# Performance work log

Hardware: AMD Instinct MI355X
Metric: run time of the kernel (lower is better)

## Reference

```python
import jax, jax.numpy as jnp
import numpy as np

B, T, C = 4, 2048, 1024
H = 16
HD = C // H  # 64


def setup_inputs() -> dict:
    key = jax.random.key(0)
    ks = jax.random.split(key, 5)
    x = jax.random.normal(ks[0], (B, T, C), dtype=jnp.float32)
    # torch nn.Linear weights have shape [out_features, in_features]
    s = 1.0 / np.sqrt(C)
    Wq = jax.random.uniform(ks[1], (C, C), jnp.float32, -s, s)
    Wk = jax.random.uniform(ks[2], (C, C), jnp.float32, -s, s)
    Wv = jax.random.uniform(ks[3], (C, C), jnp.float32, -s, s)
    Wo = jax.random.uniform(ks[4], (C, C), jnp.float32, -s, s)
    return {"x": x, "Wq": Wq, "Wk": Wk, "Wv": Wv, "Wo": Wo}


def _split_heads(t):
    b, s, c = t.shape
    return t.reshape(b, s, H, HD).transpose(0, 2, 1, 3)  # [B,H,T,HD]


def reference(x, Wq, Wk, Wv, Wo):
    q = _split_heads(x @ Wq.T)
    k = _split_heads(x @ Wk.T)
    v = _split_heads(x @ Wv.T)
    scale = 1.0 / np.sqrt(HD).astype(np.float32)
    scores = jnp.einsum('bhqd,bhkd->bhqk', q, k) * scale  # [B,H,T,T]
    causal = jnp.tril(jnp.ones((T, T), dtype=bool))
    scores = jnp.where(causal[None, None], scores, -jnp.inf)
    weights = jax.nn.softmax(scores, axis=-1)
    ctx = jnp.einsum('bhqk,bhkd->bhqd', weights, v)
    y = ctx.transpose(0, 2, 1, 3).reshape(x.shape[0], x.shape[1], C)
    return y @ Wo.T
```

## Files before the change

kernel.cpp:

```cpp
#include <hip/hip_runtime.h>

typedef __attribute__((ext_vector_type(8))) short short8;
typedef __attribute__((ext_vector_type(4))) float floatx4;

__device__ __forceinline__ ushort f2bf(float f) {
  unsigned u = __float_as_uint(f);
  u += 0x7fffu + ((u >> 16) & 1u);
  return (ushort)(u >> 16);
}

__device__ __forceinline__ uint2 pack4(floatx4 v, float scale) {
  unsigned p0 = __float_as_uint(v[0] * scale) + 0x8000u;
  unsigned p1 = __float_as_uint(v[1] * scale) + 0x8000u;
  unsigned p2 = __float_as_uint(v[2] * scale) + 0x8000u;
  unsigned p3 = __float_as_uint(v[3] * scale) + 0x8000u;
  uint2 w;
  w.x = __builtin_amdgcn_perm(p1, p0, 0x07060302);
  w.y = __builtin_amdgcn_perm(p3, p2, 0x07060302);
  return w;
}

__device__ __forceinline__ void gll16(const ushort* g, ushort* l) {
  __builtin_amdgcn_global_load_lds(
      (const __attribute__((address_space(1))) unsigned int*)(g),
      (__attribute__((address_space(3))) unsigned int*)(l), 16, 0, 0);
}

__global__ void cvt_all(const float* __restrict__ x, const float* __restrict__ a,
                        const float* __restrict__ b, const float* __restrict__ c,
                        const float* __restrict__ d, ushort* __restrict__ ox,
                        ushort* __restrict__ oa, ushort* __restrict__ ob,
                        ushort* __restrict__ oc, ushort* __restrict__ od) {
  int bid = blockIdx.x;
  const float* in;
  ushort* out;
  int lb;
  if (bid < 8192) { in = x; out = ox; lb = bid; }
  else {
    int w = (bid - 8192) >> 10;
    lb = (bid - 8192) & 1023;
    in = w == 0 ? a : (w == 1 ? b : (w == 2 ? c : d));
    out = w == 0 ? oa : (w == 1 ? ob : (w == 2 ? oc : od));
  }
  int i = (lb * 256 + threadIdx.x) * 4;
  float4 v = *(const float4*)(in + i);
  ushort4 o = make_ushort4(f2bf(v.x), f2bf(v.y), f2bf(v.z), f2bf(v.w));
  *(ushort4*)(out + i) = o;
}

__device__ __forceinline__ void stage64(const ushort* __restrict__ G, size_t gstride,
                                        int grow0, int gcol0, ushort* __restrict__ S,
                                        int wave, int lane) {
  int r8 = lane >> 3;
  int sc = ((lane & 7) ^ (r8 & 7)) * 8;
  for (int c = 0; c < 4; c++) {
    int rl = wave * 32 + c * 8;
    gll16(&G[(size_t)(grow0 + rl + r8) * gstride + gcol0 + sc], &S[rl * 64]);
  }
}

__global__ __launch_bounds__(256) void gemm_qk(const ushort* __restrict__ A,
                                               const ushort* __restrict__ W0,
                                               const ushort* __restrict__ W1,
                                               ushort* __restrict__ Qb,
                                               ushort* __restrict__ Kb) {
  __shared__ __align__(16) ushort sA[128 * 64];
  __shared__ __align__(16) ushort sB[128 * 64];
  const int K = 1024;
  int tid = threadIdx.x, wave = tid >> 6, lane = tid & 63;
  int ln = lane & 15, quad = lane >> 4;
  int m0 = blockIdx.y * 128;
  int n0g = blockIdx.x * 128;
  int mat = n0g >> 10;
  int n0 = n0g & 1023;
  const ushort* Bw = mat == 0 ? W0 : W1;

  floatx4 acc[4][4];
  for (int i = 0; i < 4; i++)
    for (int t = 0; t < 4; t++) acc[i][t] = (floatx4)0.0f;
  int mrow = (wave >> 1) * 64, ncol = (wave & 1) * 64;

  for (int k0 = 0; k0 < K; k0 += 64) {
    __syncthreads();
    stage64(A, K, m0, k0, sA, wave, lane);
    stage64(Bw, K, n0, k0, sB, wave, lane);
    __syncthreads();
    for (int ks = 0; ks < 2; ks++) {
      int cs = ((ks * 4 + quad) ^ (ln & 7)) * 8;
      short8 af[4], bf[4];
      for (int i = 0; i < 4; i++) af[i] = *(const short8*)&sB[(ncol + i * 16 + ln) * 64 + cs];
      for (int t = 0; t < 4; t++) bf[t] = *(const short8*)&sA[(mrow + t * 16 + ln) * 64 + cs];
      for (int i = 0; i < 4; i++)
        for (int t = 0; t < 4; t++)
          acc[i][t] = __builtin_amdgcn_mfma_f32_16x16x32_bf16(af[i], bf[t], acc[i][t], 0, 0, 0);
    }
  }

  float qs = (mat == 0) ? 0.18033688f : 1.0f;
  ushort* dst = (mat == 0) ? Qb : Kb;
  for (int i = 0; i < 4; i++) {
    for (int t = 0; t < 4; t++) {
      int n = n0 + ncol + i * 16 + quad * 4;
      int m = m0 + mrow + t * 16 + ln;
      int b = m >> 11, tt = m & 2047, h = n >> 6, hd = n & 63;
      *(uint2*)&dst[((((size_t)b * 16 + h) * 2048 + tt) << 6) + hd] = pack4(acc[i][t], qs);
    }
  }
}

__global__ __launch_bounds__(256) void gemm_v(const ushort* __restrict__ A,
                                              const ushort* __restrict__ W2,
                                              ushort* __restrict__ VT) {
  __shared__ __align__(16) ushort sA[128 * 64];
  __shared__ __align__(16) ushort sB[128 * 64];
  const int K = 1024;
  int tid = threadIdx.x, wave = tid >> 6, lane = tid & 63;
  int ln = lane & 15, quad = lane >> 4;
  int m0 = blockIdx.y * 128;
  int n0 = blockIdx.x * 128;

  floatx4 acc[4][4];
  for (int i = 0; i < 4; i++)
    for (int t = 0; t < 4; t++) acc[i][t] = (floatx4)0.0f;
  int mrow = (wave >> 1) * 64, ncol = (wave & 1) * 64;

  for (int k0 = 0; k0 < K; k0 += 64) {
    __syncthreads();
    stage64(A, K, m0, k0, sA, wave, lane);
    stage64(W2, K, n0, k0, sB, wave, lane);
    __syncthreads();
    for (int ks = 0; ks < 2; ks++) {
      int cs = ((ks * 4 + quad) ^ (ln & 7)) * 8;
      short8 af[4], bf[4];
      for (int i = 0; i < 4; i++) af[i] = *(const short8*)&sA[(mrow + i * 16 + ln) * 64 + cs];
      for (int t = 0; t < 4; t++) bf[t] = *(const short8*)&sB[(ncol + t * 16 + ln) * 64 + cs];
      for (int i = 0; i < 4; i++)
        for (int t = 0; t < 4; t++)
          acc[i][t] = __builtin_amdgcn_mfma_f32_16x16x32_bf16(af[i], bf[t], acc[i][t], 0, 0, 0);
    }
  }

  for (int i = 0; i < 4; i++) {
    for (int t = 0; t < 4; t++) {
      int m = m0 + mrow + i * 16 + quad * 4;
      int n = n0 + ncol + t * 16 + ln;
      int b = m >> 11, tt = m & 2047, h = n >> 6, hd = n & 63;
      *(uint2*)&VT[(((size_t)b * 16 + h) * 64 + hd) * 2048 + tt] = pack4(acc[i][t], 1.0f);
    }
  }
}

__global__ __launch_bounds__(256) void gemm_out(const ushort* __restrict__ A,
                                                const ushort* __restrict__ W0,
                                                float* __restrict__ Fout) {
  __shared__ __align__(16) ushort sA[128 * 64];
  __shared__ __align__(16) ushort sB[128 * 64];
  const int K = 1024;
  int tid = threadIdx.x, wave = tid >> 6, lane = tid & 63;
  int ln = lane & 15, quad = lane >> 4;
  int m0 = blockIdx.y * 128;
  int n0 = blockIdx.x * 128;

  floatx4 acc[4][4];
  for (int i = 0; i < 4; i++)
    for (int t = 0; t < 4; t++) acc[i][t] = (floatx4)0.0f;
  int mrow = (wave >> 1) * 64, ncol = (wave & 1) * 64;

  for (int k0 = 0; k0 < K; k0 += 64) {
    __syncthreads();
    stage64(A, K, m0, k0, sA, wave, lane);
    stage64(W0, K, n0, k0, sB, wave, lane);
    __syncthreads();
    for (int ks = 0; ks < 2; ks++) {
      int cs = ((ks * 4 + quad) ^ (ln & 7)) * 8;
      short8 af[4], bf[4];
      for (int i = 0; i < 4; i++) af[i] = *(const short8*)&sB[(ncol + i * 16 + ln) * 64 + cs];
      for (int t = 0; t < 4; t++) bf[t] = *(const short8*)&sA[(mrow + t * 16 + ln) * 64 + cs];
      for (int i = 0; i < 4; i++)
        for (int t = 0; t < 4; t++)
          acc[i][t] = __builtin_amdgcn_mfma_f32_16x16x32_bf16(af[i], bf[t], acc[i][t], 0, 0, 0);
    }
  }

  for (int i = 0; i < 4; i++) {
    for (int t = 0; t < 4; t++) {
      int n = n0 + ncol + i * 16 + quad * 4;
      int m = m0 + mrow + t * 16 + ln;
      *(floatx4*)&Fout[(size_t)m * 1024 + n] = acc[i][t];
    }
  }
}

#define SD 76
__global__ __launch_bounds__(256) void attn(const ushort* __restrict__ Qb,
                                            const ushort* __restrict__ Kb,
                                            const ushort* __restrict__ VTb,
                                            ushort* __restrict__ ctx) {
  __shared__ __align__(16) ushort sK[64 * 64];
  __shared__ __align__(16) ushort sVT[64 * 64];
  __shared__ __align__(16) ushort sP[128 * SD];

  int tid = threadIdx.x, wave = tid >> 6, lane = tid & 63;
  int ln = lane & 15, quad = lane >> 4;
  int bh = blockIdx.x;
  int qb = 15 - blockIdx.y;

  const ushort* Qp = Qb + (size_t)bh * 2048 * 64 + (size_t)qb * 128 * 64;
  const ushort* Kp = Kb + (size_t)bh * 2048 * 64;
  const ushort* VTp = VTb + (size_t)bh * 64 * 2048;

  for (int i = 0; i < 4; i++) {
    int e = tid + i * 256;
    int row = e >> 3, c8 = (e & 7) * 8;
    *(uint4*)&sP[row * SD + c8] = *(const uint4*)&Qp[row * 64 + c8];
  }
  __syncthreads();
  short8 qf[2][2];
  for (int f = 0; f < 2; f++)
    for (int ks = 0; ks < 2; ks++)
      qf[f][ks] = *(const short8*)&sP[(wave * 32 + f * 16 + ln) * SD + ks * 32 + quad * 8];

  floatx4 o[2][4];
  for (int f = 0; f < 2; f++)
    for (int t = 0; t < 4; t++) o[f][t] = (floatx4)0.0f;
  float l_acc[2] = {0.0f, 0.0f};

  int kt_m = 2 * qb + (wave >> 1);
  int ktend = 2 * qb + 1;
  int r8 = lane >> 3;
  int scs = ((lane & 7) ^ (r8 & 7)) * 8;

  for (int kt = 0; kt <= ktend; kt++) {
    __syncthreads();
    for (int c = 0; c < 2; c++) {
      int rl = wave * 16 + c * 8;
      gll16(&Kp[(size_t)(kt * 64 + rl + r8) * 64 + scs], &sK[rl * 64]);
      gll16(&VTp[(size_t)(rl + r8) * 2048 + kt * 64 + scs], &sVT[rl * 64]);
    }
    __syncthreads();
    if (kt > kt_m) continue;

    floatx4 s[2][4];
    for (int f = 0; f < 2; f++)
      for (int t = 0; t < 4; t++) s[f][t] = (floatx4)0.0f;
    for (int ks = 0; ks < 2; ks++) {
      int cs = ((ks * 4 + quad) ^ (ln & 7)) * 8;
      short8 kf[4];
      for (int t = 0; t < 4; t++)
        kf[t] = *(const short8*)&sK[(t * 16 + ln) * 64 + cs];
      for (int f = 0; f < 2; f++)
        for (int t = 0; t < 4; t++)
          s[f][t] = __builtin_amdgcn_mfma_f32_16x16x32_bf16(kf[t], qf[f][ks], s[f][t], 0, 0, 0);
    }

    if (kt == kt_m) {
      for (int f = 0; f < 2; f++) {
        int qg = qb * 128 + wave * 32 + f * 16 + ln;
        for (int t = 0; t < 4; t++) {
          int kg = kt * 64 + t * 16 + quad * 4;
          for (int r = 0; r < 4; r++)
            if (kg + r > qg) s[f][t][r] = -1e30f;
        }
      }
    }

    for (int f = 0; f < 2; f++) {
      int prow = (wave * 32 + f * 16 + ln) * SD;
      for (int t = 0; t < 4; t++) {
        floatx4 p;
        for (int r = 0; r < 4; r++) {
          p[r] = __builtin_amdgcn_exp2f(s[f][t][r]);
          l_acc[f] += p[r];
        }
        *(uint2*)&sP[prow + t * 16 + quad * 4] = pack4(p, 1.0f);
      }
    }

    for (int ks = 0; ks < 2; ks++) {
      int cs = ((ks * 4 + quad) ^ (ln & 7)) * 8;
      short8 vf[4];
      for (int t = 0; t < 4; t++)
        vf[t] = *(const short8*)&sVT[(t * 16 + ln) * 64 + cs];
      for (int f = 0; f < 2; f++) {
        short8 pf = *(const short8*)&sP[(wave * 32 + f * 16 + ln) * SD + ks * 32 + quad * 8];
        for (int t = 0; t < 4; t++)
          o[f][t] = __builtin_amdgcn_mfma_f32_16x16x32_bf16(pf, vf[t], o[f][t], 0, 0, 0);
      }
    }
  }

  for (int f = 0; f < 2; f++) {
    l_acc[f] += __shfl_xor(l_acc[f], 16);
    l_acc[f] += __shfl_xor(l_acc[f], 32);
  }

  int b = bh >> 4, h = bh & 15;
  for (int f = 0; f < 2; f++) {
    for (int r = 0; r < 4; r++) {
      float lr = __shfl(l_acc[f], quad * 4 + r);
      float linv = 1.0f / lr;
      int qg = qb * 128 + wave * 32 + f * 16 + quad * 4 + r;
      for (int t = 0; t < 4; t++) {
        int col = h * 64 + t * 16 + ln;
        ctx[((size_t)b * 2048 + qg) * 1024 + col] = f2bf(o[f][t][r] * linv);
      }
    }
  }
}

extern "C" void kernel_launch(void* const* d_in, const int* in_sizes, int n_in,
                              void* d_out, int out_size, void* d_ws, size_t ws_size,
                              hipStream_t stream) {
  const float* x  = (const float*)d_in[0];
  const float* Wq = (const float*)d_in[1];
  const float* Wk = (const float*)d_in[2];
  const float* Wv = (const float*)d_in[3];
  const float* Wo = (const float*)d_in[4];
  float* out = (float*)d_out;

  char* ws = (char*)d_ws;
  const size_t MB = 1024 * 1024;
  ushort* xb   = (ushort*)(ws + 0);
  ushort* Wqb  = (ushort*)(ws + 16 * MB);
  ushort* Wkb  = (ushort*)(ws + 18 * MB);
  ushort* Wvb  = (ushort*)(ws + 20 * MB);
  ushort* Wob  = (ushort*)(ws + 22 * MB);
  ushort* Qb   = (ushort*)(ws + 24 * MB);
  ushort* Kb   = (ushort*)(ws + 40 * MB);
  ushort* Vtb  = (ushort*)(ws + 56 * MB);
  ushort* ctxb = xb;

  cvt_all<<<12288, 256, 0, stream>>>(x, Wq, Wk, Wv, Wo, xb, Wqb, Wkb, Wvb, Wob);

  gemm_qk<<<dim3(16, 64), 256, 0, stream>>>(xb, Wqb, Wkb, Qb, Kb);
  gemm_v<<<dim3(8, 64), 256, 0, stream>>>(xb, Wvb, Vtb);
  attn<<<dim3(64, 16), 256, 0, stream>>>(Qb, Kb, Vtb, ctxb);
  gemm_out<<<dim3(8, 64), 256, 0, stream>>>(ctxb, Wob, out);
}
```

Before: 263.6 us.

## Merge QK and V projections into one kernel and remap block scheduling

Fuses the Q/K and V projection GEMMs into a single launch that picks the weight matrix and output layout per block. All grids become 1D, with the M index varying fastest so blocks running together share weight tiles. The attention grid is remapped so consecutive blocks alternate long and short causal query tiles across heads, to balance load across CUs. This saves one launch and the tail gap between kernels, at the cost of a runtime branch on the operand pointers and the epilogue.

```diff
diff --git a/kernel.cpp b/kernel.cpp
--- a/kernel.cpp
+++ b/kernel.cpp
@@ -59,31 +59,96 @@
   }
 }
 
-__global__ __launch_bounds__(256) void gemm_qk(const ushort* __restrict__ A,
-                                               const ushort* __restrict__ W0,
-                                               const ushort* __restrict__ W1,
-                                               ushort* __restrict__ Qb,
-                                               ushort* __restrict__ Kb) {
+__global__ __launch_bounds__(256) void gemm_qkv(const ushort* __restrict__ A,
+                                                const ushort* __restrict__ W0,
+                                                const ushort* __restrict__ W1,
+                                                const ushort* __restrict__ W2,
+                                                ushort* __restrict__ Qb,
+                                                ushort* __restrict__ Kb,
+                                                ushort* __restrict__ VT) {
   __shared__ __align__(16) ushort sA[128 * 64];
   __shared__ __align__(16) ushort sB[128 * 64];
   const int K = 1024;
   int tid = threadIdx.x, wave = tid >> 6, lane = tid & 63;
   int ln = lane & 15, quad = lane >> 4;
-  int m0 = blockIdx.y * 128;
-  int n0g = blockIdx.x * 128;
-  int mat = n0g >> 10;
-  int n0 = n0g & 1023;
-  const ushort* Bw = mat == 0 ? W0 : W1;
+  int bid = blockIdx.x;
+  int mblk = bid & 63, nblk = bid >> 6;
+  int m0 = mblk * 128;
+  int mat = nblk >> 3;
+  int n0 = (nblk & 7) * 128;
+  const ushort* Bw = mat == 0 ? W0 : (mat == 1 ? W1 : W2);
+  bool qkpath = (mat < 2);
 
   floatx4 acc[4][4];
   for (int i = 0; i < 4; i++)
     for (int t = 0; t < 4; t++) acc[i][t] = (floatx4)0.0f;
   int mrow = (wave >> 1) * 64, ncol = (wave & 1) * 64;
 
+  const ushort* PA = qkpath ? sB : sA;
+  const ushort* PB = qkpath ? sA : sB;
+  int aoff = qkpath ? ncol : mrow;
+  int boff = qkpath ? mrow : ncol;
+
   for (int k0 = 0; k0 < K; k0 += 64) {
     __syncthreads();
     stage64(A, K, m0, k0, sA, wave, lane);
     stage64(Bw, K, n0, k0, sB, wave, lane);
+    __syncthreads();
+    for (int ks = 0; ks < 2; ks++) {
+      int cs = ((ks * 4 + quad) ^ (ln & 7)) * 8;
+      short8 af[4], bf[4];
+      for (int i = 0; i < 4; i++) af[i] = *(const short8*)&PA[(aoff + i * 16 + ln) * 64 + cs];
+      for (int t = 0; t < 4; t++) bf[t] = *(const short8*)&PB[(boff + t * 16 + ln) * 64 + cs];
+      for (int i = 0; i < 4; i++)
+        for (int t = 0; t < 4; t++)
+          acc[i][t] = __builtin_amdgcn_mfma_f32_16x16x32_bf16(af[i], bf[t], acc[i][t], 0, 0, 0);
+    }
+  }
+
+  if (qkpath) {
+    float qs = (mat == 0) ? 0.18033688f : 1.0f;
+    ushort* dst = (mat == 0) ? Qb : Kb;
+    for (int i = 0; i < 4; i++) {
+      for (int t = 0; t < 4; t++) {
+        int n = n0 + ncol + i * 16 + quad * 4;
+        int m = m0 + mrow + t * 16 + ln;
+        int b = m >> 11, tt = m & 2047, h = n >> 6, hd = n & 63;
+        *(uint2*)&dst[((((size_t)b * 16 + h) * 2048 + tt) << 6) + hd] = pack4(acc[i][t], qs);
+      }
+    }
+  } else {
+    for (int i = 0; i < 4; i++) {
+      for (int t = 0; t < 4; t++) {
+        int m = m0 + mrow + i * 16 + quad * 4;
+        int n = n0 + ncol + t * 16 + ln;
+        int b = m >> 11, tt = m & 2047, h = n >> 6, hd = n & 63;
+        *(uint2*)&VT[(((size_t)b * 16 + h) * 64 + hd) * 2048 + tt] = pack4(acc[i][t], 1.0f);
+      }
+    }
+  }
+}
+
+__global__ __launch_bounds__(256) void gemm_out(const ushort* __restrict__ A,
+                                                const ushort* __restrict__ W0,
+                                                float* __restrict__ Fout) {
+  __shared__ __align__(16) ushort sA[128 * 64];
+  __shared__ __align__(16) ushort sB[128 * 64];
+  const int K = 1024;
+  int tid = threadIdx.x, wave = tid >> 6, lane = tid & 63;
+  int ln = lane & 15, quad = lane >> 4;
+  int bid = blockIdx.x;
+  int m0 = (bid & 63) * 128;
+  int n0 = (bid >> 6) * 128;
+
+  floatx4 acc[4][4];
+  for (int i = 0; i < 4; i++)
+    for (int t = 0; t < 4; t++) acc[i][t] = (floatx4)0.0f;
+  int mrow = (wave >> 1) * 64, ncol = (wave & 1) * 64;
+
+  for (int k0 = 0; k0 < K; k0 += 64) {
+    __syncthreads();
+    stage64(A, K, m0, k0, sA, wave, lane);
+    stage64(W0, K, n0, k0, sB, wave, lane);
     __syncthreads();
     for (int ks = 0; ks < 2; ks++) {
       int cs = ((ks * 4 + quad) ^ (ln & 7)) * 8;
@@ -96,92 +161,6 @@
     }
   }
 
-  float qs = (mat == 0) ? 0.18033688f : 1.0f;
-  ushort* dst = (mat == 0) ? Qb : Kb;
-  for (int i = 0; i < 4; i++) {
-    for (int t = 0; t < 4; t++) {
-      int n = n0 + ncol + i * 16 + quad * 4;
-      int m = m0 + mrow + t * 16 + ln;
-      int b = m >> 11, tt = m & 2047, h = n >> 6, hd = n & 63;
-      *(uint2*)&dst[((((size_t)b * 16 + h) * 2048 + tt) << 6) + hd] = pack4(acc[i][t], qs);
-    }
-  }
-}
-
-__global__ __launch_bounds__(256) void gemm_v(const ushort* __restrict__ A,
-                                              const ushort* __restrict__ W2,
-                                              ushort* __restrict__ VT) {
-  __shared__ __align__(16) ushort sA[128 * 64];
-  __shared__ __align__(16) ushort sB[128 * 64];
-  const int K = 1024;
-  int tid = threadIdx.x, wave = tid >> 6, lane = tid & 63;
-  int ln = lane & 15, quad = lane >> 4;
-  int m0 = blockIdx.y * 128;
-  int n0 = blockIdx.x * 128;
-
-  floatx4 acc[4][4];
-  for (int i = 0; i < 4; i++)
-    for (int t = 0; t < 4; t++) acc[i][t] = (floatx4)0.0f;
-  int mrow = (wave >> 1) * 64, ncol = (wave & 1) * 64;
-
-  for (int k0 = 0; k0 < K; k0 += 64) {
-    __syncthreads();
-    stage64(A, K, m0, k0, sA, wave, lane);
-    stage64(W2, K, n0, k0, sB, wave, lane);
-    __syncthreads();
-    for (int ks = 0; ks < 2; ks++) {
-      int cs = ((ks * 4 + quad) ^ (ln & 7)) * 8;
-      short8 af[4], bf[4];
-      for (int i = 0; i < 4; i++) af[i] = *(const short8*)&sA[(mrow + i * 16 + ln) * 64 + cs];
-      for (int t = 0; t < 4; t++) bf[t] = *(const short8*)&sB[(ncol + t * 16 + ln) * 64 + cs];
-      for (int i = 0; i < 4; i++)
-        for (int t = 0; t < 4; t++)
-          acc[i][t] = __builtin_amdgcn_mfma_f32_16x16x32_bf16(af[i], bf[t], acc[i][t], 0, 0, 0);
-    }
-  }
-
-  for (int i = 0; i < 4; i++) {
-    for (int t = 0; t < 4; t++) {
-      int m = m0 + mrow + i * 16 + quad * 4;
-      int n = n0 + ncol + t * 16 + ln;
-      int b = m >> 11, tt = m & 2047, h = n >> 6, hd = n & 63;
-      *(uint2*)&VT[(((size_t)b * 16 + h) * 64 + hd) * 2048 + tt] = pack4(acc[i][t], 1.0f);
-    }
-  }
-}
-
-__global__ __launch_bounds__(256) void gemm_out(const ushort* __restrict__ A,
-                                                const ushort* __restrict__ W0,
-                                                float* __restrict__ Fout) {
-  __shared__ __align__(16) ushort sA[128 * 64];
-  __shared__ __align__(16) ushort sB[128 * 64];
-  const int K = 1024;
-  int tid = threadIdx.x, wave = tid >> 6, lane = tid & 63;
-  int ln = lane & 15, quad = lane >> 4;
-  int m0 = blockIdx.y * 128;
-  int n0 = blockIdx.x * 128;
-
-  floatx4 acc[4][4];
-  for (int i = 0; i < 4; i++)
-    for (int t = 0; t < 4; t++) acc[i][t] = (floatx4)0.0f;
-  int mrow = (wave >> 1) * 64, ncol = (wave & 1) * 64;
-
-  for (int k0 = 0; k0 < K; k0 += 64) {
-    __syncthreads();
-    stage64(A, K, m0, k0, sA, wave, lane);
-    stage64(W0, K, n0, k0, sB, wave, lane);
-    __syncthreads();
-    for (int ks = 0; ks < 2; ks++) {
-      int cs = ((ks * 4 + quad) ^ (ln & 7)) * 8;
-      short8 af[4], bf[4];
-      for (int i = 0; i < 4; i++) af[i] = *(const short8*)&sB[(ncol + i * 16 + ln) * 64 + cs];
-      for (int t = 0; t < 4; t++) bf[t] = *(const short8*)&sA[(mrow + t * 16 + ln) * 64 + cs];
-      for (int i = 0; i < 4; i++)
-        for (int t = 0; t < 4; t++)
-          acc[i][t] = __builtin_amdgcn_mfma_f32_16x16x32_bf16(af[i], bf[t], acc[i][t], 0, 0, 0);
-    }
-  }
-
   for (int i = 0; i < 4; i++) {
     for (int t = 0; t < 4; t++) {
       int n = n0 + ncol + i * 16 + quad * 4;
@@ -202,8 +181,11 @@
 
   int tid = threadIdx.x, wave = tid >> 6, lane = tid & 63;
   int ln = lane & 15, quad = lane >> 4;
-  int bh = blockIdx.x;
-  int qb = 15 - blockIdx.y;
+  int bid = blockIdx.x;
+  int r = bid & 7, j = bid >> 3;
+  int zi = j & 15;
+  int qb = (zi & 1) ? (zi >> 1) : (15 - (zi >> 1));
+  int bh = (j >> 4) * 8 + r;
 
   const ushort* Qp = Qb + (size_t)bh * 2048 * 64 + (size_t)qb * 128 * 64;
   const ushort* Kp = Kb + (size_t)bh * 2048 * 64;
@@ -258,8 +240,8 @@
         int qg = qb * 128 + wave * 32 + f * 16 + ln;
         for (int t = 0; t < 4; t++) {
           int kg = kt * 64 + t * 16 + quad * 4;
-          for (int r = 0; r < 4; r++)
-            if (kg + r > qg) s[f][t][r] = -1e30f;
+          for (int r2 = 0; r2 < 4; r2++)
+            if (kg + r2 > qg) s[f][t][r2] = -1e30f;
         }
       }
     }
@@ -268,9 +250,9 @@
       int prow = (wave * 32 + f * 16 + ln) * SD;
       for (int t = 0; t < 4; t++) {
         floatx4 p;
-        for (int r = 0; r < 4; r++) {
-          p[r] = __builtin_amdgcn_exp2f(s[f][t][r]);
-          l_acc[f] += p[r];
+        for (int r2 = 0; r2 < 4; r2++) {
+          p[r2] = __builtin_amdgcn_exp2f(s[f][t][r2]);
+          l_acc[f] += p[r2];
         }
         *(uint2*)&sP[prow + t * 16 + quad * 4] = pack4(p, 1.0f);
       }
@@ -296,13 +278,13 @@
 
   int b = bh >> 4, h = bh & 15;
   for (int f = 0; f < 2; f++) {
-    for (int r = 0; r < 4; r++) {
-      float lr = __shfl(l_acc[f], quad * 4 + r);
+    for (int r2 = 0; r2 < 4; r2++) {
+      float lr = __shfl(l_acc[f], quad * 4 + r2);
       float linv = 1.0f / lr;
-      int qg = qb * 128 + wave * 32 + f * 16 + quad * 4 + r;
+      int qg = qb * 128 + wave * 32 + f * 16 + quad * 4 + r2;
       for (int t = 0; t < 4; t++) {
         int col = h * 64 + t * 16 + ln;
-        ctx[((size_t)b * 2048 + qg) * 1024 + col] = f2bf(o[f][t][r] * linv);
+        ctx[((size_t)b * 2048 + qg) * 1024 + col] = f2bf(o[f][t][r2] * linv);
       }
     }
   }
@@ -332,8 +314,7 @@
 
   cvt_all<<<12288, 256, 0, stream>>>(x, Wq, Wk, Wv, Wo, xb, Wqb, Wkb, Wvb, Wob);
 
-  gemm_qk<<<dim3(16, 64), 256, 0, stream>>>(xb, Wqb, Wkb, Qb, Kb);
-  gemm_v<<<dim3(8, 64), 256, 0, stream>>>(xb, Wvb, Vtb);
-  attn<<<dim3(64, 16), 256, 0, stream>>>(Qb, Kb, Vtb, ctxb);
-  gemm_out<<<dim3(8, 64), 256, 0, stream>>>(ctxb, Wob, out);
-}
+  gemm_qkv<<<1536, 256, 0, stream>>>(xb, Wqb, Wkb, Wvb, Qb, Kb, Vtb);
+  attn<<<1024, 256, 0, stream>>>(Qb, Kb, Vtb, ctxb);
+  gemm_out<<<512, 256, 0, stream>>>(ctxb, Wob, out);
+}
```

New measurement: 278.7 us. +5.7%, slower.
